# Performance work log

Hardware: AMD Instinct MI355X
Metric: run time of the kernel (lower is better)

The kernel has to match this reference:

```python
import jax, jax.numpy as jnp
import numpy as np

B, T, C, H = 4, 2048, 768, 12
D = C // H  # head dim = 64


def setup_inputs() -> dict:
    key = jax.random.key(0)
    ks = jax.random.split(key, 4)
    scale = 0.02
    return {
        "x": jax.random.normal(ks[0], (B, T, C), dtype=jnp.float32),
        "W_attn": jax.random.normal(ks[1], (C, 3 * C), dtype=jnp.float32) * scale,
        "b_attn": jnp.zeros((3 * C,), dtype=jnp.float32),
        "W_proj": jax.random.normal(ks[2], (C, C), dtype=jnp.float32) * scale,
        "b_proj": jnp.zeros((C,), dtype=jnp.float32),
    }


def reference(x, W_attn, b_attn, W_proj, b_proj):
    Bsz, Tlen, Cdim = x.shape
    qkv = x @ W_attn + b_attn                    # [B,T,3C]
    q, k, v = jnp.split(qkv, 3, axis=-1)          # each [B,T,C]
    # [B,T,C] -> [B,H,T,D]
    def heads(t):
        return t.reshape(Bsz, Tlen, H, D).transpose(0, 2, 1, 3)
    q, k, v = heads(q), heads(k), heads(v)
    att = jnp.einsum("bhqd,bhkd->bhqk", q, k) * (1.0 / np.sqrt(D))
    # causal mask: position q attends to k <= q
    mask = jnp.tril(jnp.ones((Tlen, Tlen), dtype=bool))
    att = jnp.where(mask[None, None], att, -jnp.inf)
    att = jax.nn.softmax(att, axis=-1)
    y = jnp.einsum("bhqk,bhkd->bhqd", att, v)     # [B,H,T,D]
    y = y.transpose(0, 2, 1, 3).reshape(Bsz, Tlen, Cdim)
    return y @ W_proj + b_proj
```

## Files before the change

kernel.cpp:

```cpp
#include <hip/hip_runtime.h>

#define B_SZ   4
#define T_LEN  2048
#define C_DIM  768
#define H_NUM  12
#define THREEC (3 * C_DIM)
#define M_ROWS (B_SZ * T_LEN)
#define CAST_N8 (M_ROWS * C_DIM / 8)
#define CAST_BLOCKS (CAST_N8 / 256)
#define TP_BX ((THREEC + C_DIM) / 32)
#define TP_BY (C_DIM / 32)

typedef _Float16 f16;
typedef _Float16 half8 __attribute__((ext_vector_type(8)));
typedef _Float16 half4 __attribute__((ext_vector_type(4)));
typedef __fp16   pk2   __attribute__((ext_vector_type(2)));
typedef float    f32x4 __attribute__((ext_vector_type(4)));

#define GLD16(gaddr, laddr)                                                         \
  __builtin_amdgcn_global_load_lds(                                                 \
      (const __attribute__((address_space(1))) unsigned int*)(gaddr),               \
      (__attribute__((address_space(3))) unsigned int*)(laddr), 16, 0, 0)
#define MFMA16(a, b, c) __builtin_amdgcn_mfma_f32_16x16x32_f16(a, b, c, 0, 0, 0)

__global__ __launch_bounds__(256) void prep_kernel(
    const float* __restrict__ x, f16* __restrict__ xh,
    const float* __restrict__ Wa, const float* __restrict__ Wp,
    f16* __restrict__ WtA, f16* __restrict__ WtP) {
  __shared__ f16 tile[32][33];
  const int bid = blockIdx.x;
  if (bid < CAST_BLOCKS) {
    int i = bid * 256 + threadIdx.x;
    const float* s = x + (size_t)i * 8;
    half8 h;
#pragma unroll
    for (int u = 0; u < 8; ++u) h[u] = (f16)s[u];
    *(half8*)(xh + (size_t)i * 8) = h;
    return;
  }
  const int t = bid - CAST_BLOCKS;
  int bx = t % TP_BX;
  const int by = t / TP_BX;
  const float* W; f16* Wt; int N;
  if (bx < THREEC / 32) { W = Wa; Wt = WtA; N = THREEC; }
  else { W = Wp; Wt = WtP; N = C_DIM; bx -= THREEC / 32; }
  const int n0 = bx * 32, k0 = by * 32;
  const int tx = threadIdx.x & 31, ty = threadIdx.x >> 5;
#pragma unroll
  for (int i = 0; i < 4; ++i)
    tile[ty + i * 8][tx] = (f16)W[(size_t)(k0 + ty + i * 8) * N + n0 + tx];
  __syncthreads();
#pragma unroll
  for (int i = 0; i < 4; ++i)
    Wt[(size_t)(n0 + ty + i * 8) * C_DIM + k0 + tx] = tile[tx][ty + i * 8];
}

template <int BM, int BN, int OUT_F16, int SWZ>
__global__ __launch_bounds__(256) void gemm_f16_kernel(
    const f16* __restrict__ A, const f16* __restrict__ Bt,
    const float* __restrict__ bias, f16* __restrict__ OutH,
    float* __restrict__ OutF, int M, int N, int K) {
  __shared__ f16 As[BM * 64];
  __shared__ f16 Bs[BN * 64];
  const int tid = threadIdx.x;
  const int lane = tid & 63, wave = tid >> 6;
  const int lm = lane & 15, kq = lane >> 4, lm7 = lm & 7;
  constexpr int MT = BM / 32, NT = BN / 32;
  const int wm = (wave & 1) * (BM / 2), wn = (wave >> 1) * (BN / 2);

  int bx = blockIdx.x, by = blockIdx.y;
  if (SWZ) {
    const int nx = gridDim.x;
    const int lin = by * nx + bx;
    const int cpx = (nx * gridDim.y) >> 3;
    const int swz = (lin & 7) * cpx + (lin >> 3);
    bx = swz % nx;
    by = swz / nx;
  }
  const int row0 = by * BM, col0 = bx * BN;

  f32x4 acc[MT][NT] = {};

  for (int k0 = 0; k0 < K; k0 += 64) {
    __syncthreads();
#pragma unroll
    for (int i = 0; i < BM / 32; ++i) {
      int c = tid + i * 256;
      int r = c >> 3, cc = (c & 7) ^ (r & 7);
      GLD16(&A[(size_t)(row0 + r) * K + k0 + cc * 8],
            &As[(i * 256 + wave * 64) * 8]);
    }
#pragma unroll
    for (int i = 0; i < BN / 32; ++i) {
      int c = tid + i * 256;
      int r = c >> 3, cc = (c & 7) ^ (r & 7);
      GLD16(&Bt[(size_t)(col0 + r) * K + k0 + cc * 8],
            &Bs[(i * 256 + wave * 64) * 8]);
    }
    __syncthreads();
#pragma unroll
    for (int ks = 0; ks < 2; ++ks) {
      const int pos = (ks * 4 + kq);
      half8 af[MT], bf[NT];
#pragma unroll
      for (int t = 0; t < MT; ++t)
        af[t] = *(const half8*)&As[(wm + t * 16 + lm) * 64 + (pos ^ lm7) * 8];
#pragma unroll
      for (int t = 0; t < NT; ++t)
        bf[t] = *(const half8*)&Bs[(wn + t * 16 + lm) * 64 + (pos ^ lm7) * 8];
#pragma unroll
      for (int mt = 0; mt < MT; ++mt)
#pragma unroll
        for (int nt = 0; nt < NT; ++nt)
          acc[mt][nt] = MFMA16(af[mt], bf[nt], acc[mt][nt]);
    }
  }

#pragma unroll
  for (int mt = 0; mt < MT; ++mt) {
    const int row = row0 + wm + mt * 16 + kq * 4;
#pragma unroll
    for (int nt = 0; nt < NT; ++nt) {
      const int col = col0 + wn + nt * 16 + lm;
      const float bv = bias[col];
#pragma unroll
      for (int r = 0; r < 4; ++r) {
        float v = acc[mt][nt][r] + bv;
        if (OUT_F16)
          OutH[(size_t)(row + r) * N + col] = (f16)v;
        else
          OutF[(size_t)(row + r) * N + col] = v;
      }
    }
  }
}

__global__ __launch_bounds__(256) void v_transpose_kernel(
    const f16* __restrict__ qkv, f16* __restrict__ vt) {
  __shared__ f16 tile[64 * 68];
  const int bh = blockIdx.x, b = bh / H_NUM, h = bh % H_NUM;
  const int t0 = blockIdx.y * 64;
  const int tid = threadIdx.x;
#pragma unroll
  for (int i = 0; i < 2; ++i) {
    int c = tid + i * 256;
    int tr = c >> 3, doff = (c & 7) * 8;
    int pcol = ((tr >> 5) << 5) | (((tr >> 2) & 3) << 3) |
               (((tr >> 4) & 1) << 2) | (tr & 3);
    half8 v = *(const half8*)&qkv[(size_t)(b * T_LEN + t0 + tr) * THREEC + 2 * C_DIM + h * 64 + doff];
#pragma unroll
    for (int u = 0; u < 8; ++u) tile[(doff + u) * 68 + pcol] = v[u];
  }
  __syncthreads();
#pragma unroll
  for (int i = 0; i < 2; ++i) {
    int c = tid + i * 256;
    int d = c >> 3, toff = (c & 7) * 8;
    half8 v;
#pragma unroll
    for (int u = 0; u < 8; ++u) v[u] = tile[d * 68 + toff + u];
    *(half8*)&vt[((size_t)bh * 64 + d) * T_LEN + t0 + toff] = v;
  }
}

__global__ __launch_bounds__(512, 8) void attn_kernel(
    const f16* __restrict__ qkv, const f16* __restrict__ vt,
    f16* __restrict__ y) {
  __shared__ f16 Kt[2][64 * 64];
  __shared__ f16 Vt[2][64 * 64];

  const int bh = blockIdx.x, b = bh / H_NUM, h = bh % H_NUM;
  const int yb = blockIdx.y;
  const int qb = 15 - yb;
  const int tid = threadIdx.x, lane = tid & 63, wave = tid >> 6;
  const int lm = lane & 15, kq = lane >> 4, lm7 = lm & 7;
  const int cw = qb * 2 + (wave >> 2);
  const int qw = cw * 64 + (wave & 3) * 16;
  const f16 qscale = (f16)(0.125f * 1.44269504f);

  half8 vones;
#pragma unroll
  for (int u = 0; u < 8; ++u) vones[u] = (f16)1.f;

  half8 bq[2];
#pragma unroll
  for (int c2 = 0; c2 < 2; ++c2) {
    half8 v = *(const half8*)&qkv[(size_t)(b * T_LEN + qw + lm) * THREEC +
                                  h * 64 + c2 * 32 + kq * 8];
    bq[c2] = v * qscale;
  }

  f32x4 o[4] = {};
  f32x4 ol = {};

  f32x4 fz = {};
  asm volatile("" : "+v"(fz));

  const int srow = tid >> 3;
  const int scol = ((tid & 7) ^ (srow & 7)) * 8;
  const f16* kp = &qkv[(size_t)(b * T_LEN + srow) * THREEC + C_DIM + h * 64 + scol];
  const f16* vp = &vt[((size_t)bh * 64 + srow) * T_LEN + scol];

  const int sbase = wave * 512;

  const int n_tiles = qb * 2 + 2;

  GLD16(kp, &Kt[0][sbase]);
  kp += (size_t)64 * THREEC;
  GLD16(vp, &Vt[0][sbase]);
  vp += 64;

  for (int it = 0; it < n_tiles; ++it) {
    const int cur = it & 1;
    if (it + 1 < n_tiles) {
      GLD16(kp, &Kt[cur ^ 1][sbase]);
      kp += (size_t)64 * THREEC;
      GLD16(vp, &Vt[cur ^ 1][sbase]);
      vp += 64;
      asm volatile("s_waitcnt vmcnt(2)" ::: "memory");
    } else {
      asm volatile("s_waitcnt vmcnt(0)" ::: "memory");
    }
    __builtin_amdgcn_s_barrier();

    if (it <= cw) {
      f32x4 s4[4];
#pragma unroll
      for (int ct = 0; ct < 4; ++ct) {
        const f16* kr = &Kt[cur][(ct * 16 + lm) * 64];
        half8 ak0 = *(const half8*)&kr[(kq ^ lm7) * 8];
        half8 ak1 = *(const half8*)&kr[((4 + kq) ^ lm7) * 8];
        f32x4 z = MFMA16(ak0, bq[0], fz);
        s4[ct] = MFMA16(ak1, bq[1], z);
      }
      if (it == cw) {
        const int qrow = qw + lm, j0 = it * 64;
#pragma unroll
        for (int ct = 0; ct < 4; ++ct)
#pragma unroll
          for (int r = 0; r < 4; ++r)
            if (j0 + ct * 16 + kq * 4 + r > qrow) s4[ct][r] = -1e30f;
      }
      union { half8 h8; pk2 p2[4]; } pa0, pa1;
      pa0.p2[0] = __builtin_amdgcn_cvt_pkrtz(
          __builtin_amdgcn_exp2f(s4[0][0]), __builtin_amdgcn_exp2f(s4[0][1]));
      pa0.p2[1] = __builtin_amdgcn_cvt_pkrtz(
          __builtin_amdgcn_exp2f(s4[0][2]), __builtin_amdgcn_exp2f(s4[0][3]));
      pa0.p2[2] = __builtin_amdgcn_cvt_pkrtz(
          __builtin_amdgcn_exp2f(s4[1][0]), __builtin_amdgcn_exp2f(s4[1][1]));
      pa0.p2[3] = __builtin_amdgcn_cvt_pkrtz(
          __builtin_amdgcn_exp2f(s4[1][2]), __builtin_amdgcn_exp2f(s4[1][3]));
      pa1.p2[0] = __builtin_amdgcn_cvt_pkrtz(
          __builtin_amdgcn_exp2f(s4[2][0]), __builtin_amdgcn_exp2f(s4[2][1]));
      pa1.p2[1] = __builtin_amdgcn_cvt_pkrtz(
          __builtin_amdgcn_exp2f(s4[2][2]), __builtin_amdgcn_exp2f(s4[2][3]));
      pa1.p2[2] = __builtin_amdgcn_cvt_pkrtz(
          __builtin_amdgcn_exp2f(s4[3][0]), __builtin_amdgcn_exp2f(s4[3][1]));
      pa1.p2[3] = __builtin_amdgcn_cvt_pkrtz(
          __builtin_amdgcn_exp2f(s4[3][2]), __builtin_amdgcn_exp2f(s4[3][3]));

#pragma unroll
      for (int dt = 0; dt < 4; ++dt) {
        const f16* vr = &Vt[cur][(dt * 16 + lm) * 64];
        half8 bv0 = *(const half8*)&vr[(kq ^ lm7) * 8];
        half8 bv1 = *(const half8*)&vr[((4 + kq) ^ lm7) * 8];
        o[dt] = MFMA16(pa0.h8, bv0, o[dt]);
        o[dt] = MFMA16(pa1.h8, bv1, o[dt]);
      }
      ol = MFMA16(pa0.h8, vones, ol);
      ol = MFMA16(pa1.h8, vones, ol);
    }

    __builtin_amdgcn_s_barrier();
  }

#pragma unroll
  for (int r = 0; r < 4; ++r) {
    const float inv = 1.f / ol[r];
    const size_t base =
        (size_t)(b * T_LEN + qw + kq * 4 + r) * C_DIM + h * 64;
#pragma unroll
    for (int dt = 0; dt < 4; ++dt)
      y[base + dt * 16 + lm] = (f16)(o[dt][r] * inv);
  }
}

extern "C" void kernel_launch(void* const* d_in, const int* in_sizes, int n_in,
                              void* d_out, int out_size, void* d_ws, size_t ws_size,
                              hipStream_t stream) {
  const float* x      = (const float*)d_in[0];
  const float* W_attn = (const float*)d_in[1];
  const float* b_attn = (const float*)d_in[2];
  const float* W_proj = (const float*)d_in[3];
  const float* b_proj = (const float*)d_in[4];
  float* out = (float*)d_out;

  const int M = M_ROWS;
  auto align256 = [](size_t v) { return (v + 255) & ~(size_t)255; };
  char* ws = (char*)d_ws;
  f16* xh   = (f16*)ws; ws += align256((size_t)M * C_DIM * 2);
  f16* WtA  = (f16*)ws; ws += align256((size_t)THREEC * C_DIM * 2);
  f16* WtP  = (f16*)ws; ws += align256((size_t)C_DIM * C_DIM * 2);
  f16* qkvh = (f16*)ws; ws += align256((size_t)M * THREEC * 2);
  f16* vtg  = (f16*)ws; ws += align256((size_t)B_SZ * H_NUM * 64 * T_LEN * 2);
  f16* yh   = (f16*)ws; ws += align256((size_t)M * C_DIM * 2);

  prep_kernel<<<CAST_BLOCKS + TP_BX * TP_BY, 256, 0, stream>>>(
      x, xh, W_attn, W_proj, WtA, WtP);

  gemm_f16_kernel<128, 128, 1, 1><<<dim3(THREEC / 128, M / 128), 256, 0, stream>>>(
      xh, WtA, b_attn, qkvh, nullptr, M, THREEC, C_DIM);

  v_transpose_kernel<<<dim3(B_SZ * H_NUM, T_LEN / 64), 256, 0, stream>>>(qkvh, vtg);

  attn_kernel<<<dim3(B_SZ * H_NUM, 16), 512, 0, stream>>>(qkvh, vtg, yh);

  gemm_f16_kernel<128, 64, 0, 1><<<dim3(C_DIM / 64, M / 128), 256, 0, stream>>>(
      yh, WtP, b_proj, nullptr, out, M, C_DIM, C_DIM);
}
```

Baseline: 191.3 us.

## Give each attention wave two 16-row query tiles with 256-thread blocks

Attention blocks shrink from 8 waves to 4, and each wave now processes 32 query rows as two 16-row MFMA tiles. Each K/V fragment read from LDS is reused for both tiles, and each thread issues two global-to-LDS loads per tile instead of one. This halves LDS read traffic per MFMA and barrier participants per block, at the cost of more accumulator registers and a lower occupancy hint in the launch bounds.

```diff
diff --git a/kernel.cpp b/kernel.cpp
--- a/kernel.cpp
+++ b/kernel.cpp
@@ -163,7 +163,7 @@
   }
 }
 
-__global__ __launch_bounds__(512, 8) void attn_kernel(
+__global__ __launch_bounds__(256, 3) void attn_kernel(
     const f16* __restrict__ qkv, const f16* __restrict__ vt,
     f16* __restrict__ y) {
   __shared__ f16 Kt[2][64 * 64];
@@ -174,24 +174,26 @@
   const int qb = 15 - yb;
   const int tid = threadIdx.x, lane = tid & 63, wave = tid >> 6;
   const int lm = lane & 15, kq = lane >> 4, lm7 = lm & 7;
-  const int cw = qb * 2 + (wave >> 2);
-  const int qw = cw * 64 + (wave & 3) * 16;
+  const int cw = qb * 2 + (wave >> 1);
+  const int qw = qb * 128 + wave * 32;
   const f16 qscale = (f16)(0.125f * 1.44269504f);
 
   half8 vones;
 #pragma unroll
   for (int u = 0; u < 8; ++u) vones[u] = (f16)1.f;
 
-  half8 bq[2];
-#pragma unroll
-  for (int c2 = 0; c2 < 2; ++c2) {
-    half8 v = *(const half8*)&qkv[(size_t)(b * T_LEN + qw + lm) * THREEC +
-                                  h * 64 + c2 * 32 + kq * 8];
-    bq[c2] = v * qscale;
-  }
-
-  f32x4 o[4] = {};
-  f32x4 ol = {};
+  half8 bq[2][2];
+#pragma unroll
+  for (int cq = 0; cq < 2; ++cq)
+#pragma unroll
+    for (int c2 = 0; c2 < 2; ++c2) {
+      half8 v = *(const half8*)&qkv[(size_t)(b * T_LEN + qw + cq * 16 + lm) * THREEC +
+                                    h * 64 + c2 * 32 + kq * 8];
+      bq[cq][c2] = v * qscale;
+    }
+
+  f32x4 o[4][2] = {};
+  f32x4 ol[2] = {};
 
   f32x4 fz = {};
   asm volatile("" : "+v"(fz));
@@ -200,89 +202,113 @@
   const int scol = ((tid & 7) ^ (srow & 7)) * 8;
   const f16* kp = &qkv[(size_t)(b * T_LEN + srow) * THREEC + C_DIM + h * 64 + scol];
   const f16* vp = &vt[((size_t)bh * 64 + srow) * T_LEN + scol];
+  const size_t kp2 = (size_t)32 * THREEC;
+  const size_t vp2 = (size_t)32 * T_LEN;
 
   const int sbase = wave * 512;
 
   const int n_tiles = qb * 2 + 2;
 
   GLD16(kp, &Kt[0][sbase]);
+  GLD16(kp + kp2, &Kt[0][2048 + sbase]);
+  GLD16(vp, &Vt[0][sbase]);
+  GLD16(vp + vp2, &Vt[0][2048 + sbase]);
   kp += (size_t)64 * THREEC;
-  GLD16(vp, &Vt[0][sbase]);
   vp += 64;
 
   for (int it = 0; it < n_tiles; ++it) {
     const int cur = it & 1;
     if (it + 1 < n_tiles) {
       GLD16(kp, &Kt[cur ^ 1][sbase]);
+      GLD16(kp + kp2, &Kt[cur ^ 1][2048 + sbase]);
+      GLD16(vp, &Vt[cur ^ 1][sbase]);
+      GLD16(vp + vp2, &Vt[cur ^ 1][2048 + sbase]);
       kp += (size_t)64 * THREEC;
-      GLD16(vp, &Vt[cur ^ 1][sbase]);
       vp += 64;
-      asm volatile("s_waitcnt vmcnt(2)" ::: "memory");
+      asm volatile("s_waitcnt vmcnt(4)" ::: "memory");
     } else {
       asm volatile("s_waitcnt vmcnt(0)" ::: "memory");
     }
     __builtin_amdgcn_s_barrier();
 
     if (it <= cw) {
-      f32x4 s4[4];
+      f32x4 s4[4][2];
 #pragma unroll
       for (int ct = 0; ct < 4; ++ct) {
         const f16* kr = &Kt[cur][(ct * 16 + lm) * 64];
         half8 ak0 = *(const half8*)&kr[(kq ^ lm7) * 8];
         half8 ak1 = *(const half8*)&kr[((4 + kq) ^ lm7) * 8];
-        f32x4 z = MFMA16(ak0, bq[0], fz);
-        s4[ct] = MFMA16(ak1, bq[1], z);
+#pragma unroll
+        for (int cq = 0; cq < 2; ++cq) {
+          f32x4 z = MFMA16(ak0, bq[cq][0], fz);
+          s4[ct][cq] = MFMA16(ak1, bq[cq][1], z);
+        }
       }
       if (it == cw) {
-        const int qrow = qw + lm, j0 = it * 64;
+        const int j0 = it * 64;
 #pragma unroll
         for (int ct = 0; ct < 4; ++ct)
 #pragma unroll
-          for (int r = 0; r < 4; ++r)
-            if (j0 + ct * 16 + kq * 4 + r > qrow) s4[ct][r] = -1e30f;
-      }
-      union { half8 h8; pk2 p2[4]; } pa0, pa1;
-      pa0.p2[0] = __builtin_amdgcn_cvt_pkrtz(
-          __builtin_amdgcn_exp2f(s4[0][0]), __builtin_amdgcn_exp2f(s4[0][1]));
-      pa0.p2[1] = __builtin_amdgcn_cvt_pkrtz(
-          __builtin_amdgcn_exp2f(s4[0][2]), __builtin_amdgcn_exp2f(s4[0][3]));
-      pa0.p2[2] = __builtin_amdgcn_cvt_pkrtz(
-          __builtin_amdgcn_exp2f(s4[1][0]), __builtin_amdgcn_exp2f(s4[1][1]));
-      pa0.p2[3] = __builtin_amdgcn_cvt_pkrtz(
-          __builtin_amdgcn_exp2f(s4[1][2]), __builtin_amdgcn_exp2f(s4[1][3]));
-      pa1.p2[0] = __builtin_amdgcn_cvt_pkrtz(
-          __builtin_amdgcn_exp2f(s4[2][0]), __builtin_amdgcn_exp2f(s4[2][1]));
-      pa1.p2[1] = __builtin_amdgcn_cvt_pkrtz(
-          __builtin_amdgcn_exp2f(s4[2][2]), __builtin_amdgcn_exp2f(s4[2][3]));
-      pa1.p2[2] = __builtin_amdgcn_cvt_pkrtz(
-          __builtin_amdgcn_exp2f(s4[3][0]), __builtin_amdgcn_exp2f(s4[3][1]));
-      pa1.p2[3] = __builtin_amdgcn_cvt_pkrtz(
-          __builtin_amdgcn_exp2f(s4[3][2]), __builtin_amdgcn_exp2f(s4[3][3]));
+          for (int cq = 0; cq < 2; ++cq) {
+            const int qrow = qw + cq * 16 + lm;
+#pragma unroll
+            for (int r = 0; r < 4; ++r)
+              if (j0 + ct * 16 + kq * 4 + r > qrow) s4[ct][cq][r] = -1e30f;
+          }
+      }
+      union { half8 h8; pk2 p2[4]; } pa0[2], pa1[2];
+#pragma unroll
+      for (int cq = 0; cq < 2; ++cq) {
+        pa0[cq].p2[0] = __builtin_amdgcn_cvt_pkrtz(
+            __builtin_amdgcn_exp2f(s4[0][cq][0]), __builtin_amdgcn_exp2f(s4[0][cq][1]));
+        pa0[cq].p2[1] = __builtin_amdgcn_cvt_pkrtz(
+            __builtin_amdgcn_exp2f(s4[0][cq][2]), __builtin_amdgcn_exp2f(s4[0][cq][3]));
+        pa0[cq].p2[2] = __builtin_amdgcn_cvt_pkrtz(
+            __builtin_amdgcn_exp2f(s4[1][cq][0]), __builtin_amdgcn_exp2f(s4[1][cq][1]));
+        pa0[cq].p2[3] = __builtin_amdgcn_cvt_pkrtz(
+            __builtin_amdgcn_exp2f(s4[1][cq][2]), __builtin_amdgcn_exp2f(s4[1][cq][3]));
+        pa1[cq].p2[0] = __builtin_amdgcn_cvt_pkrtz(
+            __builtin_amdgcn_exp2f(s4[2][cq][0]), __builtin_amdgcn_exp2f(s4[2][cq][1]));
+        pa1[cq].p2[1] = __builtin_amdgcn_cvt_pkrtz(
+            __builtin_amdgcn_exp2f(s4[2][cq][2]), __builtin_amdgcn_exp2f(s4[2][cq][3]));
+        pa1[cq].p2[2] = __builtin_amdgcn_cvt_pkrtz(
+            __builtin_amdgcn_exp2f(s4[3][cq][0]), __builtin_amdgcn_exp2f(s4[3][cq][1]));
+        pa1[cq].p2[3] = __builtin_amdgcn_cvt_pkrtz(
+            __builtin_amdgcn_exp2f(s4[3][cq][2]), __builtin_amdgcn_exp2f(s4[3][cq][3]));
+      }
 
 #pragma unroll
       for (int dt = 0; dt < 4; ++dt) {
         const f16* vr = &Vt[cur][(dt * 16 + lm) * 64];
         half8 bv0 = *(const half8*)&vr[(kq ^ lm7) * 8];
         half8 bv1 = *(const half8*)&vr[((4 + kq) ^ lm7) * 8];
-        o[dt] = MFMA16(pa0.h8, bv0, o[dt]);
-        o[dt] = MFMA16(pa1.h8, bv1, o[dt]);
-      }
-      ol = MFMA16(pa0.h8, vones, ol);
-      ol = MFMA16(pa1.h8, vones, ol);
+#pragma unroll
+        for (int cq = 0; cq < 2; ++cq) {
+          o[dt][cq] = MFMA16(pa0[cq].h8, bv0, o[dt][cq]);
+          o[dt][cq] = MFMA16(pa1[cq].h8, bv1, o[dt][cq]);
+        }
+      }
+#pragma unroll
+      for (int cq = 0; cq < 2; ++cq) {
+        ol[cq] = MFMA16(pa0[cq].h8, vones, ol[cq]);
+        ol[cq] = MFMA16(pa1[cq].h8, vones, ol[cq]);
+      }
     }
 
     __builtin_amdgcn_s_barrier();
   }
 
 #pragma unroll
-  for (int r = 0; r < 4; ++r) {
-    const float inv = 1.f / ol[r];
-    const size_t base =
-        (size_t)(b * T_LEN + qw + kq * 4 + r) * C_DIM + h * 64;
-#pragma unroll
-    for (int dt = 0; dt < 4; ++dt)
-      y[base + dt * 16 + lm] = (f16)(o[dt][r] * inv);
-  }
+  for (int cq = 0; cq < 2; ++cq)
+#pragma unroll
+    for (int r = 0; r < 4; ++r) {
+      const float inv = 1.f / ol[cq][r];
+      const size_t base =
+          (size_t)(b * T_LEN + qw + cq * 16 + kq * 4 + r) * C_DIM + h * 64;
+#pragma unroll
+      for (int dt = 0; dt < 4; ++dt)
+        y[base + dt * 16 + lm] = (f16)(o[dt][cq][r] * inv);
+    }
 }
 
 extern "C" void kernel_launch(void* const* d_in, const int* in_sizes, int n_in,
@@ -313,7 +339,7 @@
 
   v_transpose_kernel<<<dim3(B_SZ * H_NUM, T_LEN / 64), 256, 0, stream>>>(qkvh, vtg);
 
-  attn_kernel<<<dim3(B_SZ * H_NUM, 16), 512, 0, stream>>>(qkvh, vtg, yh);
+  attn_kernel<<<dim3(B_SZ * H_NUM, 16), 256, 0, stream>>>(qkvh, vtg, yh);
 
   gemm_f16_kernel<128, 64, 0, 1><<<dim3(C_DIM / 64, M / 128), 256, 0, stream>>>(
       yh, WtP, b_proj, nullptr, out, M, C_DIM, C_DIM);
```

New measurement: 187.7 us. Within noise of the previous version (-1.9%).
